# Kernel tuning notes

Measured on AMD Instinct MI355X. Metric: run time of the kernel, lower is better.

Reference implementation:

```python
import jax, jax.numpy as jnp
import numpy as np

SCALE = 1.0


def _chamfer_pair(a, b):
    # a: [N,3], b: [M,3] -> (dist1 [N], dist2 [M]) squared NN distances
    # ||a-b||^2 = ||a||^2 + ||b||^2 - 2 a.b
    aa = jnp.sum(a * a, axis=-1)            # [N]
    bb = jnp.sum(b * b, axis=-1)            # [M]
    ab = jnp.einsum('nd,md->nm', a, b)      # [N,M]
    d = aa[:, None] + bb[None, :] - 2.0 * ab
    d = jnp.maximum(d, 0.0)
    return jnp.min(d, axis=1), jnp.min(d, axis=0)


def reference(p1, p2):
    # p1, p2: [B, N, 3]; scale applied before distance, matching the torch module
    a = p1 * SCALE
    b = p2 * SCALE
    dist1, dist2 = jax.vmap(_chamfer_pair)(a, b)  # [B,N], [B,M]
    # per-sample loss = mean(dist1) + mean(dist2); total averaged over batch
    per_sample = jnp.mean(dist1, axis=1) + jnp.mean(dist2, axis=1)  # [B]
    return jnp.mean(per_sample).reshape(1)


def setup_inputs() -> dict:
    key = jax.random.key(0)
    k1, k2 = jax.random.split(key)
    B, N, M = 4, 8192, 8192
    p1 = jax.random.normal(k1, (B, N, 3), dtype=jnp.float32)
    p2 = jax.random.normal(k2, (B, M, 3), dtype=jnp.float32)
    return {"p1": p1, "p2": p2}
```

## Files before the change

### kernel.cpp

```cpp
#include <hip/hip_runtime.h>
#include <math.h>

#define BATCH   4
#define NPTS    8192
#define THREADS 256
#define NQ      (2 * BATCH * NPTS)
#define TCH     32
#define QPT     4
#define CHUNK   (NPTS / TCH)
#define QPB     (THREADS * QPT)
#define QTILES  (NPTS / QPB)

static constexpr float SCALE = 1.0f;


__global__ __launch_bounds__(THREADS, 8)
void chamfer_min_kernel(const float* __restrict__ p1,
                        const float* __restrict__ p2,
                        unsigned* __restrict__ qmin_g,
                        float* __restrict__ acc)
{
    if (blockIdx.x == 0 && threadIdx.x < 3)
        reinterpret_cast<unsigned*>(acc)[threadIdx.x] = 0u;

    __shared__ float4 lds4[CHUNK];

    const int bid = blockIdx.x;
    const int c   = bid % TCH;
    const int qt  = (bid / TCH) % QTILES;
    const int b   = (bid / (TCH * QTILES)) % BATCH;
    const int dir = bid / (TCH * QTILES * BATCH);

    const float* qptr = (dir == 0 ? p1 : p2) + (size_t)b * NPTS * 3;
    const float* tptr = (dir == 0 ? p2 : p1) + (size_t)b * NPTS * 3;

    const float* tsrc = tptr + (size_t)c * CHUNK * 3;
    for (int i = threadIdx.x; i < CHUNK; i += THREADS) {
        const float x = tsrc[3 * i + 0] * SCALE;
        const float y = tsrc[3 * i + 1] * SCALE;
        const float z = tsrc[3 * i + 2] * SCALE;
        const float bb = fmaf(z, z, fmaf(y, y, x * x));
        lds4[i] = make_float4(-2.0f * x, -2.0f * y, -2.0f * z, bb);
    }

    const int t  = threadIdx.x;
    const int q0 = qt * QPB + t;
    float qx[QPT], qy[QPT], qz[QPT], qmin[QPT];
    #pragma unroll
    for (int k = 0; k < QPT; ++k) {
        const int q = q0 + k * THREADS;
        qx[k] = qptr[q * 3 + 0] * SCALE;
        qy[k] = qptr[q * 3 + 1] * SCALE;
        qz[k] = qptr[q * 3 + 2] * SCALE;
        qmin[k] = 3.0e38f;
    }

    __syncthreads();

    for (int j = 0; j < CHUNK; j += 8) {
        #pragma unroll
        for (int i = 0; i < 8; i += 2) {
            const float4 t0 = lds4[j + i];
            const float4 t1 = lds4[j + i + 1];
            #pragma unroll
            for (int k = 0; k < QPT; ++k) {
                float s0 = fmaf(qx[k], t0.x, t0.w);
                s0 = fmaf(qy[k], t0.y, s0);
                s0 = fmaf(qz[k], t0.z, s0);
                float s1 = fmaf(qx[k], t1.x, t1.w);
                s1 = fmaf(qy[k], t1.y, s1);
                s1 = fmaf(qz[k], t1.z, s1);
                qmin[k] = fminf(qmin[k], fminf(s0, s1));
            }
        }
    }

    #pragma unroll
    for (int k = 0; k < QPT; ++k) {
        const float aa = fmaf(qz[k], qz[k], fmaf(qy[k], qy[k], qx[k] * qx[k]));
        const int q = q0 + k * THREADS;
        float d = fmaxf(qmin[k] + aa, 0.0f);
        atomicMin(&qmin_g[(size_t)(dir * BATCH + b) * NPTS + q],
                  __float_as_uint(d));
    }
}

__global__ __launch_bounds__(THREADS)
void chamfer_reduce_kernel(const unsigned* __restrict__ qmin_g,
                           float* __restrict__ acc,
                           float* __restrict__ out)
{
    const int idx = blockIdx.x * THREADS + threadIdx.x;
    float m = __uint_as_float(qmin_g[idx]);

    #pragma unroll
    for (int o = 32; o > 0; o >>= 1) m += __shfl_down(m, o, 64);

    __shared__ float red[4];
    const int wave = threadIdx.x >> 6;
    const int lane = threadIdx.x & 63;
    if (lane == 0) red[wave] = m;
    __syncthreads();
    if (threadIdx.x == 0) {
        const float s = red[0] + red[1] + red[2] + red[3];
        atomicAdd(&acc[blockIdx.x >> 7], s);
        __threadfence();
        const unsigned tk = atomicAdd(reinterpret_cast<unsigned*>(acc + 2), 1u);
        if (tk == 255) {
            __threadfence();
            const float s0 = atomicAdd(&acc[0], 0.0f);
            const float s1 = atomicAdd(&acc[1], 0.0f);
            out[0] = (s0 + s1) * (1.0f / (float)(BATCH * NPTS));
        }
    }
}

extern "C" void kernel_launch(void* const* d_in, const int* in_sizes, int n_in,
                              void* d_out, int out_size, void* d_ws, size_t ws_size,
                              hipStream_t stream) {
    const float* p1 = (const float*)d_in[0];
    const float* p2 = (const float*)d_in[1];
    float* out = (float*)d_out;

    unsigned* qmin_g = (unsigned*)d_ws;
    float*    acc    = (float*)(qmin_g + NQ);

    chamfer_min_kernel<<<2 * BATCH * QTILES * TCH, THREADS, 0, stream>>>(p1, p2, qmin_g, acc);
    chamfer_reduce_kernel<<<NQ / THREADS, THREADS, 0, stream>>>(qmin_g, acc, out);
}
```

Measured before the change: 104.6 us.

## Compute pairwise distances with bf16 split-precision MFMA instead of scalar FMAs

Adds a prep kernel that packs each point into 16-element bf16 records. Coordinates and squared norms are split into high and low bf16 parts so that one 32x32x16 MFMA produces the full ||a||^2+||b||^2-2a·b. The main kernel stages target records in LDS and runs MFMAs per wave, reducing each query's min with fminf over the accumulator and a cross-half shuffle. This moves the O(N·M) distance work from VALU FMAs to the matrix cores, in exchange for an extra kernel launch, more workspace traffic and possible precision loss from the bf16 hi/lo split (the lo*lo cross term is dropped).

```diff
diff --git a/kernel.cpp b/kernel.cpp
--- a/kernel.cpp
+++ b/kernel.cpp
@@ -5,84 +5,126 @@
 #define NPTS    8192
 #define THREADS 256
 #define NQ      (2 * BATCH * NPTS)
-#define TCH     32
-#define QPT     4
+#define TCH     16
 #define CHUNK   (NPTS / TCH)
-#define QPB     (THREADS * QPT)
+#define QPB     128
 #define QTILES  (NPTS / QPB)
 
 static constexpr float SCALE = 1.0f;
 
+typedef __attribute__((ext_vector_type(8)))  short          bf16x8;
+typedef __attribute__((ext_vector_type(8)))  unsigned short u16x8;
+typedef __attribute__((ext_vector_type(16))) float          f32x16;
+
+__device__ __forceinline__ unsigned short f2b(float f) {
+    union { float f; unsigned u; } v; v.f = f;
+    return (unsigned short)((v.u + 0x7FFFu + ((v.u >> 16) & 1u)) >> 16);
+}
+__device__ __forceinline__ float b2f(unsigned short h) {
+    union { unsigned u; float f; } v; v.u = ((unsigned)h) << 16;
+    return v.f;
+}
+
+
+__global__ __launch_bounds__(THREADS)
+void chamfer_prep_kernel(const float* __restrict__ p1,
+                         const float* __restrict__ p2,
+                         unsigned short* __restrict__ trec,
+                         unsigned short* __restrict__ qrec,
+                         float* __restrict__ acc)
+{
+    const int id   = blockIdx.x * THREADS + threadIdx.x;
+    const int role = id >> 16;
+    const int slot = id & 65535;
+    const int dir  = slot >> 15;
+    const int rem  = slot & 32767;
+    const float* tc = (dir == 0 ? p2 : p1);
+    const float* qc = (dir == 0 ? p1 : p2);
+    const float* src = role ? qc : tc;
+
+    const float x = src[rem * 3 + 0] * SCALE;
+    const float y = src[rem * 3 + 1] * SCALE;
+    const float z = src[rem * 3 + 2] * SCALE;
+
+    unsigned short r[16];
+    const unsigned short one = 0x3F80;
+    if (role == 0) {
+        const unsigned short xh = f2b(x), yh = f2b(y), zh = f2b(z);
+        const unsigned short xl = f2b(x - b2f(xh));
+        const unsigned short yl = f2b(y - b2f(yh));
+        const unsigned short zl = f2b(z - b2f(zh));
+        const float bb = fmaf(z, z, fmaf(y, y, x * x));
+        const unsigned short bh = f2b(bb), bl = f2b(bb - b2f(bh));
+        r[0]=xh; r[1]=yh; r[2]=zh;  r[3]=xl; r[4]=yl; r[5]=zl;
+        r[6]=xh; r[7]=yh; r[8]=zh;  r[9]=bh; r[10]=bl;
+        r[11]=one; r[12]=one; r[13]=0; r[14]=0; r[15]=0;
+        u16x8* dst = (u16x8*)(trec + (size_t)slot * 16);
+        dst[0] = *(u16x8*)&r[0];
+        dst[1] = *(u16x8*)&r[8];
+    } else {
+        const float mx = -2.0f * x, my = -2.0f * y, mz = -2.0f * z;
+        const unsigned short xh = f2b(mx), yh = f2b(my), zh = f2b(mz);
+        const unsigned short xl = f2b(mx - b2f(xh));
+        const unsigned short yl = f2b(my - b2f(yh));
+        const unsigned short zl = f2b(mz - b2f(zh));
+        const float aa = fmaf(z, z, fmaf(y, y, x * x));
+        const unsigned short ah = f2b(aa), al = f2b(aa - b2f(ah));
+        r[0]=xh; r[1]=yh; r[2]=zh;  r[3]=xh; r[4]=yh; r[5]=zh;
+        r[6]=xl; r[7]=yl; r[8]=zl;  r[9]=one; r[10]=one;
+        r[11]=ah; r[12]=al; r[13]=0; r[14]=0; r[15]=0;
+        u16x8* dst = (u16x8*)(qrec + (size_t)slot * 16);
+        dst[0] = *(u16x8*)&r[0];
+        dst[1] = *(u16x8*)&r[8];
+    }
+    if (id < 3) reinterpret_cast<unsigned*>(acc)[id] = 0u;
+}
 
 __global__ __launch_bounds__(THREADS, 8)
-void chamfer_min_kernel(const float* __restrict__ p1,
-                        const float* __restrict__ p2,
-                        unsigned* __restrict__ qmin_g,
-                        float* __restrict__ acc)
+void chamfer_mfma_kernel(const unsigned short* __restrict__ trec,
+                         const unsigned short* __restrict__ qrec,
+                         unsigned* __restrict__ qmin_g)
 {
-    if (blockIdx.x == 0 && threadIdx.x < 3)
-        reinterpret_cast<unsigned*>(acc)[threadIdx.x] = 0u;
-
-    __shared__ float4 lds4[CHUNK];
+    __shared__ unsigned short lds[CHUNK * 16];
 
     const int bid = blockIdx.x;
     const int c   = bid % TCH;
     const int qt  = (bid / TCH) % QTILES;
     const int b   = (bid / (TCH * QTILES)) % BATCH;
     const int dir = bid / (TCH * QTILES * BATCH);
+    const int base = (dir * BATCH + b) * NPTS;
 
-    const float* qptr = (dir == 0 ? p1 : p2) + (size_t)b * NPTS * 3;
-    const float* tptr = (dir == 0 ? p2 : p1) + (size_t)b * NPTS * 3;
+    const u16x8* tsrc = (const u16x8*)(trec + (size_t)(base + c * CHUNK) * 16);
+    u16x8* l8 = (u16x8*)lds;
+    #pragma unroll
+    for (int i = threadIdx.x; i < CHUNK * 2; i += THREADS) l8[i] = tsrc[i];
 
-    const float* tsrc = tptr + (size_t)c * CHUNK * 3;
-    for (int i = threadIdx.x; i < CHUNK; i += THREADS) {
-        const float x = tsrc[3 * i + 0] * SCALE;
-        const float y = tsrc[3 * i + 1] * SCALE;
-        const float z = tsrc[3 * i + 2] * SCALE;
-        const float bb = fmaf(z, z, fmaf(y, y, x * x));
-        lds4[i] = make_float4(-2.0f * x, -2.0f * y, -2.0f * z, bb);
-    }
-
-    const int t  = threadIdx.x;
-    const int q0 = qt * QPB + t;
-    float qx[QPT], qy[QPT], qz[QPT], qmin[QPT];
-    #pragma unroll
-    for (int k = 0; k < QPT; ++k) {
-        const int q = q0 + k * THREADS;
-        qx[k] = qptr[q * 3 + 0] * SCALE;
-        qy[k] = qptr[q * 3 + 1] * SCALE;
-        qz[k] = qptr[q * 3 + 2] * SCALE;
-        qmin[k] = 3.0e38f;
-    }
+    const int l = threadIdx.x & 63;
+    const int w = threadIdx.x >> 6;
+    const int qslot = base + qt * QPB + w * 32 + (l & 31);
+    const bf16x8 bv = *(const bf16x8*)(qrec + ((size_t)qslot * 2 + (l >> 5)) * 8);
 
     __syncthreads();
 
-    for (int j = 0; j < CHUNK; j += 8) {
-        #pragma unroll
-        for (int i = 0; i < 8; i += 2) {
-            const float4 t0 = lds4[j + i];
-            const float4 t1 = lds4[j + i + 1];
-            #pragma unroll
-            for (int k = 0; k < QPT; ++k) {
-                float s0 = fmaf(qx[k], t0.x, t0.w);
-                s0 = fmaf(qy[k], t0.y, s0);
-                s0 = fmaf(qz[k], t0.z, s0);
-                float s1 = fmaf(qx[k], t1.x, t1.w);
-                s1 = fmaf(qy[k], t1.y, s1);
-                s1 = fmaf(qz[k], t1.z, s1);
-                qmin[k] = fminf(qmin[k], fminf(s0, s1));
-            }
-        }
+    float rm = 3.0e38f;
+    #pragma unroll 4
+    for (int tb = 0; tb < CHUNK / 32; ++tb) {
+        const bf16x8 av =
+            *(const bf16x8*)&lds[(tb * 64 + (l & 31) * 2 + (l >> 5)) * 8];
+        f32x16 zc = {0.f,0.f,0.f,0.f,0.f,0.f,0.f,0.f,
+                     0.f,0.f,0.f,0.f,0.f,0.f,0.f,0.f};
+        const f32x16 d =
+            __builtin_amdgcn_mfma_f32_32x32x16_bf16(av, bv, zc, 0, 0, 0);
+        const float f0 = fminf(fminf(d[0],  d[1]),  fminf(d[2],  d[3]));
+        const float f1 = fminf(fminf(d[4],  d[5]),  fminf(d[6],  d[7]));
+        const float f2 = fminf(fminf(d[8],  d[9]),  fminf(d[10], d[11]));
+        const float f3 = fminf(fminf(d[12], d[13]), fminf(d[14], d[15]));
+        rm = fminf(rm, fminf(fminf(f0, f1), fminf(f2, f3)));
     }
 
-    #pragma unroll
-    for (int k = 0; k < QPT; ++k) {
-        const float aa = fmaf(qz[k], qz[k], fmaf(qy[k], qy[k], qx[k] * qx[k]));
-        const int q = q0 + k * THREADS;
-        float d = fmaxf(qmin[k] + aa, 0.0f);
-        atomicMin(&qmin_g[(size_t)(dir * BATCH + b) * NPTS + q],
-                  __float_as_uint(d));
-    }
+    rm = fminf(rm, __shfl_xor(rm, 32, 64));
+    rm = fmaxf(rm, 0.0f);
+    if (l < 32)
+        atomicMin(&qmin_g[qslot], __float_as_uint(rm));
 }
 
 __global__ __launch_bounds__(THREADS)
@@ -122,9 +164,12 @@
     const float* p2 = (const float*)d_in[1];
     float* out = (float*)d_out;
 
-    unsigned* qmin_g = (unsigned*)d_ws;
-    float*    acc    = (float*)(qmin_g + NQ);
+    unsigned short* trec = (unsigned short*)d_ws;
+    unsigned short* qrec = trec + (size_t)NQ * 16;
+    unsigned*       qmin = (unsigned*)(qrec + (size_t)NQ * 16);
+    float*          acc  = (float*)(qmin + NQ);
 
-    chamfer_min_kernel<<<2 * BATCH * QTILES * TCH, THREADS, 0, stream>>>(p1, p2, qmin_g, acc);
-    chamfer_reduce_kernel<<<NQ / THREADS, THREADS, 0, stream>>>(qmin_g, acc, out);
+    chamfer_prep_kernel<<<2 * NQ / THREADS, THREADS, 0, stream>>>(p1, p2, trec, qrec, acc);
+    chamfer_mfma_kernel<<<2 * BATCH * QTILES * TCH, THREADS, 0, stream>>>(trec, qrec, qmin);
+    chamfer_reduce_kernel<<<NQ / THREADS, THREADS, 0, stream>>>(qmin, acc, out);
 }
```

Measured after the change: 92.56 us. 1.13x faster.
